# Kernel tuning notes

Hardware: AMD Instinct MI355X
Metric: run time of the kernel (lower is better)

Reference implementation:

```python
import jax, jax.numpy as jnp
import numpy as np

B, T, D, H = 64, 2048, 512, 512
NEG_INF = -1e9


def setup_inputs() -> dict:
    key = jax.random.key(0)
    k1, k2, k3 = jax.random.split(key, 3)
    x = jax.random.normal(k1, (B, D), dtype=jnp.float32)
    enc_outs = jax.random.normal(k2, (B, T, D), dtype=jnp.float32)
    # Dense(hidden) applied to concat([x, context]) -> weight [2*D, H]
    W = jax.random.normal(k3, (2 * D, H), dtype=jnp.float32) * (1.0 / np.sqrt(2 * D))
    b = jnp.zeros((H,), dtype=jnp.float32)
    actual_step = 100  # scalar step counter (int state)
    return {"x": x, "enc_outs": enc_outs, "W": W, "b": b, "actual_step": actual_step}


def reference(x, enc_outs, W, b, actual_step):
    # Dot-product attention of query x over enc_outs, masking the current step.
    # scores: [B, T]
    scores = jnp.einsum('bd,btd->bt', x, enc_outs)
    t_idx = jnp.arange(enc_outs.shape[1])
    scores = jnp.where((t_idx == actual_step)[None, :], NEG_INF, scores)
    alignment = jax.nn.softmax(scores, axis=-1)          # [B, T]
    context = jnp.einsum('bt,btd->bd', alignment, enc_outs)  # [B, D]
    # gate = sigmoid(Dense(concat([x, context])))
    att = jax.nn.sigmoid(jnp.concatenate([x, context], axis=-1) @ W + b)  # [B, H]
    content_selected = att * x                           # requires H == D
    return content_selected
```

## Files before the change

### kernel.cpp

```cpp
#include <hip/hip_runtime.h>
#include <math.h>

#define BB 64
#define TT 2048
#define DD 512
#define HH 512
#define NC 16
#define CHUNK (TT / NC)
#define TH 8.0f

__global__ __launch_bounds__(256) void k1_partial(
    const float* __restrict__ x, const float* __restrict__ enc,
    const int* __restrict__ step_ptr,
    float* __restrict__ ws_m, float* __restrict__ ws_l, float* __restrict__ ws_c)
{
    const int chunk = blockIdx.x;
    const int b     = blockIdx.y;
    const int tid   = threadIdx.x;
    const int w     = tid >> 6;
    const int lane  = tid & 63;
    const int step  = *step_ptr;
    const int trow0 = chunk * CHUNK + w * 32;

    const float4* xr = (const float4*)(x + (size_t)b * DD);
    const float4 xa = xr[lane];
    const float4 xb = xr[64 + lane];

    const float4* __restrict__ rp =
        (const float4*)(enc + (size_t)b * TT * DD) + (size_t)trow0 * 128 + lane;

    float m = -1e30f, l = 0.f;
    float4 ca = make_float4(0.f,0.f,0.f,0.f), cb = make_float4(0.f,0.f,0.f,0.f);

    float4 A[2][2], Bv[2][2];
    A[0][0]  = rp[0 * 128];      A[0][1]  = rp[1 * 128];
    Bv[0][0] = rp[0 * 128 + 64]; Bv[0][1] = rp[1 * 128 + 64];

    #pragma unroll 4
    for (int jj = 0; jj < 8; ++jj) {
        #pragma unroll
        for (int par = 0; par < 2; ++par) {
            const int bat = jj * 2 + par;
            const int nx  = par ^ 1;
            if (bat < 15) {
                A[nx][0]  = rp[((bat + 1) * 2 + 0) * 128];
                A[nx][1]  = rp[((bat + 1) * 2 + 1) * 128];
                Bv[nx][0] = rp[((bat + 1) * 2 + 0) * 128 + 64];
                Bv[nx][1] = rp[((bat + 1) * 2 + 1) * 128 + 64];
            }
            float s[2];
            #pragma unroll
            for (int r = 0; r < 2; ++r) {
                const float4 ea = A[par][r], eb = Bv[par][r];
                s[r] = ea.x*xa.x + ea.y*xa.y + ea.z*xa.z + ea.w*xa.w
                     + eb.x*xb.x + eb.y*xb.y + eb.z*xb.z + eb.w*xb.w;
            }
            #pragma unroll
            for (int off = 32; off; off >>= 1) {
                s[0] += __shfl_xor(s[0], off, 64);
                s[1] += __shfl_xor(s[1], off, 64);
            }
            #pragma unroll
            for (int r = 0; r < 2; ++r)
                if (trow0 + bat * 2 + r == step) s[r] = -1e30f;

            const float bm = fmaxf(s[0], s[1]);
            if (bm > m + TH) {
                const float sc = __expf(m - bm);
                l *= sc;
                ca.x *= sc; ca.y *= sc; ca.z *= sc; ca.w *= sc;
                cb.x *= sc; cb.y *= sc; cb.z *= sc; cb.w *= sc;
                m = bm;
            }
            const float w0 = __expf(s[0] - m);
            const float w1 = __expf(s[1] - m);
            l += w0 + w1;
            ca.x = fmaf(w0, A[par][0].x, fmaf(w1, A[par][1].x, ca.x));
            ca.y = fmaf(w0, A[par][0].y, fmaf(w1, A[par][1].y, ca.y));
            ca.z = fmaf(w0, A[par][0].z, fmaf(w1, A[par][1].z, ca.z));
            ca.w = fmaf(w0, A[par][0].w, fmaf(w1, A[par][1].w, ca.w));
            cb.x = fmaf(w0, Bv[par][0].x, fmaf(w1, Bv[par][1].x, cb.x));
            cb.y = fmaf(w0, Bv[par][0].y, fmaf(w1, Bv[par][1].y, cb.y));
            cb.z = fmaf(w0, Bv[par][0].z, fmaf(w1, Bv[par][1].z, cb.z));
            cb.w = fmaf(w0, Bv[par][0].w, fmaf(w1, Bv[par][1].w, cb.w));
        }
    }

    __shared__ float ls_m[4], ls_l[4];
    __shared__ float ls_c[4][DD];
    if (lane == 0) { ls_m[w] = m; ls_l[w] = l; }
    {
        float* cw = ls_c[w];
        const int d0 = lane * 4;
        cw[d0 + 0] = ca.x; cw[d0 + 1] = ca.y; cw[d0 + 2] = ca.z; cw[d0 + 3] = ca.w;
        cw[256 + d0 + 0] = cb.x; cw[256 + d0 + 1] = cb.y;
        cw[256 + d0 + 2] = cb.z; cw[256 + d0 + 3] = cb.w;
    }
    __syncthreads();

    const float M = fmaxf(fmaxf(ls_m[0], ls_m[1]), fmaxf(ls_m[2], ls_m[3]));
    const float f0 = __expf(ls_m[0] - M);
    const float f1 = __expf(ls_m[1] - M);
    const float f2 = __expf(ls_m[2] - M);
    const float f3 = __expf(ls_m[3] - M);
    const float L = ls_l[0] * f0 + ls_l[1] * f1 + ls_l[2] * f2 + ls_l[3] * f3;

    const int bc = b * NC + chunk;
    for (int d = tid; d < DD; d += 256) {
        const float v = ls_c[0][d] * f0 + ls_c[1][d] * f1
                      + ls_c[2][d] * f2 + ls_c[3][d] * f3;
        ws_c[(size_t)bc * DD + d] = v;
    }
    if (tid == 0) { ws_m[bc] = M; ws_l[bc] = L; }
}

__global__ __launch_bounds__(256) void k1b_merge(
    const float* __restrict__ ws_m, const float* __restrict__ ws_l,
    const float* __restrict__ ws_c, float* __restrict__ ctx)
{
    const int b    = blockIdx.x;
    const int half = blockIdx.y;
    const int tid  = threadIdx.x;
    __shared__ float fac[NC];

    float M = -1e30f;
    #pragma unroll
    for (int i = 0; i < NC; ++i) M = fmaxf(M, ws_m[b * NC + i]);
    float L = 0.f;
    #pragma unroll
    for (int i = 0; i < NC; ++i) L += ws_l[b * NC + i] * __expf(ws_m[b * NC + i] - M);
    const float inv = 1.f / L;
    if (tid < NC) fac[tid] = __expf(ws_m[b * NC + tid] - M) * inv;
    __syncthreads();

    const int d = half * 256 + tid;
    float acc = 0.f;
    #pragma unroll
    for (int i = 0; i < NC; ++i)
        acc = fmaf(ws_c[(size_t)(b * NC + i) * DD + d], fac[i], acc);
    ctx[(size_t)b * DD + d] = acc;
}

#define COLS 8
__device__ __forceinline__ int cidx(int k, int bb) {
    return (k >> 5) * 260 + (k & 31) * 8 + bb;
}

__global__ __launch_bounds__(256) void k2_gemm(
    const float* __restrict__ x, const float* __restrict__ ctx,
    const float* __restrict__ W, const float* __restrict__ bias,
    float* __restrict__ out)
{
    const int g   = blockIdx.x;
    const int bg  = blockIdx.y;
    const int tid = threadIdx.x;

    __shared__ float  con[32 * 260];
    __shared__ float4 part[4][COLS][8];

    const float4* x4 = (const float4*)x;
    const float4* c4 = (const float4*)ctx;

    for (int idx = tid; idx < 2048; idx += 256) {
        const int bb = idx >> 8, k4 = idx & 255;
        const int b  = bg * 8 + bb;
        const float4 v = (k4 < 128) ? x4[(size_t)b * 128 + k4]
                                    : c4[(size_t)b * 128 + (k4 - 128)];
        const int k = k4 * 4;
        con[cidx(k + 0, bb)] = v.x;
        con[cidx(k + 1, bb)] = v.y;
        con[cidx(k + 2, bb)] = v.z;
        con[cidx(k + 3, bb)] = v.w;
    }
    __syncthreads();

    const int cl   = tid & 7;
    const int kseg = tid >> 3;
    const int col4 = g * COLS + cl;
    const float4* Wp = (const float4*)W + (size_t)(kseg * 32) * 128 + col4;

    float4 acc[8];
    #pragma unroll
    for (int bb = 0; bb < 8; ++bb) acc[bb] = make_float4(0.f,0.f,0.f,0.f);

    #pragma unroll 4
    for (int kk = 0; kk < 32; ++kk) {
        const float4 wv = Wp[(size_t)kk * 128];
        const int k = kseg * 32 + kk;
        const float4 c0 = *(const float4*)&con[cidx(k, 0)];
        const float4 c1 = *(const float4*)&con[cidx(k, 4)];
        const float cv[8] = {c0.x, c0.y, c0.z, c0.w, c1.x, c1.y, c1.z, c1.w};
        #pragma unroll
        for (int bb = 0; bb < 8; ++bb) {
            acc[bb].x = fmaf(cv[bb], wv.x, acc[bb].x);
            acc[bb].y = fmaf(cv[bb], wv.y, acc[bb].y);
            acc[bb].z = fmaf(cv[bb], wv.z, acc[bb].z);
            acc[bb].w = fmaf(cv[bb], wv.w, acc[bb].w);
        }
    }

    #pragma unroll
    for (int off = 8; off <= 32; off <<= 1) {
        #pragma unroll
        for (int bb = 0; bb < 8; ++bb) {
            acc[bb].x += __shfl_xor(acc[bb].x, off, 64);
            acc[bb].y += __shfl_xor(acc[bb].y, off, 64);
            acc[bb].z += __shfl_xor(acc[bb].z, off, 64);
            acc[bb].w += __shfl_xor(acc[bb].w, off, 64);
        }
    }
    const int wv_ = tid >> 6, lane = tid & 63;
    if (lane < 8) {
        #pragma unroll
        for (int bb = 0; bb < 8; ++bb) part[wv_][lane][bb] = acc[bb];
    }
    __syncthreads();

    if (tid < 64) {
        const int bb = tid >> 3, cl2 = tid & 7;
        float4 r = part[0][cl2][bb];
        #pragma unroll
        for (int ww = 1; ww < 4; ++ww) {
            const float4 p = part[ww][cl2][bb];
            r.x += p.x; r.y += p.y; r.z += p.z; r.w += p.w;
        }
        const int c4i = g * COLS + cl2;
        const int h   = c4i * 4;
        const int b   = bg * 8 + bb;
        const float4 bv = ((const float4*)bias)[c4i];
        const float xv0 = con[cidx(h + 0, bb)];
        const float xv1 = con[cidx(h + 1, bb)];
        const float xv2 = con[cidx(h + 2, bb)];
        const float xv3 = con[cidx(h + 3, bb)];
        float4 o;
        o.x = xv0 / (1.f + __expf(-(r.x + bv.x)));
        o.y = xv1 / (1.f + __expf(-(r.y + bv.y)));
        o.z = xv2 / (1.f + __expf(-(r.z + bv.z)));
        o.w = xv3 / (1.f + __expf(-(r.w + bv.w)));
        ((float4*)out)[(size_t)b * 128 + c4i] = o;
    }
}

extern "C" void kernel_launch(void* const* d_in, const int* in_sizes, int n_in,
                              void* d_out, int out_size, void* d_ws, size_t ws_size,
                              hipStream_t stream) {
    const float* x    = (const float*)d_in[0];
    const float* enc  = (const float*)d_in[1];
    const float* W    = (const float*)d_in[2];
    const float* bias = (const float*)d_in[3];
    const int*   step = (const int*)d_in[4];
    float* out = (float*)d_out;
    float* ws  = (float*)d_ws;

    float* ws_m = ws;
    float* ws_l = ws_m + (size_t)BB * NC;
    float* ws_c = ws_l + (size_t)BB * NC;
    float* ctx  = ws_c + (size_t)BB * NC * DD;

    k1_partial<<<dim3(NC, BB), 256, 0, stream>>>(x, enc, step, ws_m, ws_l, ws_c);
    k1b_merge<<<dim3(BB, 2), 256, 0, stream>>>(ws_m, ws_l, ws_c, ctx);
    k2_gemm<<<dim3(16, 8), 256, 0, stream>>>(x, ctx, W, bias, out);
}
```

Measured before the change: 62.28 us.

## Stream encoder rows through LDS with async global_load_lds ring buffer

Replaces the register double-buffered float4 loads of encoder rows with a 4-deep per-wave LDS ring filled by global_load_lds direct-to-LDS transfers, keeping three rows in flight and synchronising with explicit s_waitcnt vmcnt counts. Rows are now consumed one at a time instead of in pairs. The goal is deeper memory-level parallelism for this bandwidth-bound streaming pass. In exchange it adds 32KB of LDS per block, which may reduce occupancy, adds LDS read traffic, and relies on hand-written waitcnt counts whose correctness depends on compiler load ordering.

```diff
diff --git a/kernel.cpp b/kernel.cpp
--- a/kernel.cpp
+++ b/kernel.cpp
@@ -8,6 +8,14 @@
 #define NC 16
 #define CHUNK (TT / NC)
 #define TH 8.0f
+
+typedef unsigned int u32;
+__device__ __forceinline__ void async_load16(const float* g, float* l) {
+    __builtin_amdgcn_global_load_lds(
+        (const __attribute__((address_space(1))) u32*)g,
+        (__attribute__((address_space(3))) u32*)l,
+        16, 0, 0);
+}
 
 __global__ __launch_bounds__(256) void k1_partial(
     const float* __restrict__ x, const float* __restrict__ enc,
@@ -22,72 +30,67 @@
     const int step  = *step_ptr;
     const int trow0 = chunk * CHUNK + w * 32;
 
+    __shared__ float stage[4][4][DD];
+    __shared__ float ls_m[4], ls_l[4];
+    __shared__ float ls_c[4][DD];
+
     const float4* xr = (const float4*)(x + (size_t)b * DD);
     const float4 xa = xr[lane];
     const float4 xb = xr[64 + lane];
-
-    const float4* __restrict__ rp =
-        (const float4*)(enc + (size_t)b * TT * DD) + (size_t)trow0 * 128 + lane;
+    asm volatile("s_waitcnt vmcnt(0)" ::: "memory");
+
+    const float* gbase = enc + (size_t)b * TT * DD + (size_t)trow0 * DD;
 
     float m = -1e30f, l = 0.f;
     float4 ca = make_float4(0.f,0.f,0.f,0.f), cb = make_float4(0.f,0.f,0.f,0.f);
 
-    float4 A[2][2], Bv[2][2];
-    A[0][0]  = rp[0 * 128];      A[0][1]  = rp[1 * 128];
-    Bv[0][0] = rp[0 * 128 + 64]; Bv[0][1] = rp[1 * 128 + 64];
-
-    #pragma unroll 4
-    for (int jj = 0; jj < 8; ++jj) {
-        #pragma unroll
-        for (int par = 0; par < 2; ++par) {
-            const int bat = jj * 2 + par;
-            const int nx  = par ^ 1;
-            if (bat < 15) {
-                A[nx][0]  = rp[((bat + 1) * 2 + 0) * 128];
-                A[nx][1]  = rp[((bat + 1) * 2 + 1) * 128];
-                Bv[nx][0] = rp[((bat + 1) * 2 + 0) * 128 + 64];
-                Bv[nx][1] = rp[((bat + 1) * 2 + 1) * 128 + 64];
-            }
-            float s[2];
-            #pragma unroll
-            for (int r = 0; r < 2; ++r) {
-                const float4 ea = A[par][r], eb = Bv[par][r];
-                s[r] = ea.x*xa.x + ea.y*xa.y + ea.z*xa.z + ea.w*xa.w
-                     + eb.x*xb.x + eb.y*xb.y + eb.z*xb.z + eb.w*xb.w;
-            }
-            #pragma unroll
-            for (int off = 32; off; off >>= 1) {
-                s[0] += __shfl_xor(s[0], off, 64);
-                s[1] += __shfl_xor(s[1], off, 64);
-            }
-            #pragma unroll
-            for (int r = 0; r < 2; ++r)
-                if (trow0 + bat * 2 + r == step) s[r] = -1e30f;
-
-            const float bm = fmaxf(s[0], s[1]);
-            if (bm > m + TH) {
-                const float sc = __expf(m - bm);
-                l *= sc;
-                ca.x *= sc; ca.y *= sc; ca.z *= sc; ca.w *= sc;
-                cb.x *= sc; cb.y *= sc; cb.z *= sc; cb.w *= sc;
-                m = bm;
-            }
-            const float w0 = __expf(s[0] - m);
-            const float w1 = __expf(s[1] - m);
-            l += w0 + w1;
-            ca.x = fmaf(w0, A[par][0].x, fmaf(w1, A[par][1].x, ca.x));
-            ca.y = fmaf(w0, A[par][0].y, fmaf(w1, A[par][1].y, ca.y));
-            ca.z = fmaf(w0, A[par][0].z, fmaf(w1, A[par][1].z, ca.z));
-            ca.w = fmaf(w0, A[par][0].w, fmaf(w1, A[par][1].w, ca.w));
-            cb.x = fmaf(w0, Bv[par][0].x, fmaf(w1, Bv[par][1].x, cb.x));
-            cb.y = fmaf(w0, Bv[par][0].y, fmaf(w1, Bv[par][1].y, cb.y));
-            cb.z = fmaf(w0, Bv[par][0].z, fmaf(w1, Bv[par][1].z, cb.z));
-            cb.w = fmaf(w0, Bv[par][0].w, fmaf(w1, Bv[par][1].w, cb.w));
-        }
-    }
-
-    __shared__ float ls_m[4], ls_l[4];
-    __shared__ float ls_c[4][DD];
+    #define ISSUE(r) {                                              \
+        const float* g_ = gbase + (r) * DD + lane * 4;              \
+        float* d_ = &stage[w][(r) & 3][0];                          \
+        async_load16(g_, d_);                                       \
+        async_load16(g_ + 256, d_ + 256);                           \
+    }
+    #define CONSUME(r) {                                            \
+        const float* sp_ = &stage[w][(r) & 3][0];                   \
+        const float4 ea = *(const float4*)&sp_[lane * 4];           \
+        const float4 eb = *(const float4*)&sp_[256 + lane * 4];     \
+        float s = ea.x*xa.x + ea.y*xa.y + ea.z*xa.z + ea.w*xa.w     \
+                + eb.x*xb.x + eb.y*xb.y + eb.z*xb.z + eb.w*xb.w;    \
+        _Pragma("unroll")                                           \
+        for (int off = 32; off; off >>= 1) s += __shfl_xor(s, off, 64); \
+        if (trow0 + (r) == step) s = -1e30f;                        \
+        if (s > m + TH) {                                           \
+            const float sc_ = __expf(m - s);                        \
+            l *= sc_;                                               \
+            ca.x *= sc_; ca.y *= sc_; ca.z *= sc_; ca.w *= sc_;     \
+            cb.x *= sc_; cb.y *= sc_; cb.z *= sc_; cb.w *= sc_;     \
+            m = s;                                                  \
+        }                                                           \
+        const float wgt = __expf(s - m);                            \
+        l += wgt;                                                   \
+        ca.x = fmaf(wgt, ea.x, ca.x); ca.y = fmaf(wgt, ea.y, ca.y); \
+        ca.z = fmaf(wgt, ea.z, ca.z); ca.w = fmaf(wgt, ea.w, ca.w); \
+        cb.x = fmaf(wgt, eb.x, cb.x); cb.y = fmaf(wgt, eb.y, cb.y); \
+        cb.z = fmaf(wgt, eb.z, cb.z); cb.w = fmaf(wgt, eb.w, cb.w); \
+    }
+
+    ISSUE(0); ISSUE(1); ISSUE(2);
+
+    for (int r = 0; r < 29; ++r) {
+        ISSUE(r + 3);
+        asm volatile("s_waitcnt vmcnt(6)" ::: "memory");
+        CONSUME(r);
+    }
+    asm volatile("s_waitcnt vmcnt(4)" ::: "memory");
+    CONSUME(29);
+    asm volatile("s_waitcnt vmcnt(2)" ::: "memory");
+    CONSUME(30);
+    asm volatile("s_waitcnt vmcnt(0)" ::: "memory");
+    CONSUME(31);
+
+    #undef ISSUE
+    #undef CONSUME
+
     if (lane == 0) { ls_m[w] = m; ls_l[w] = l; }
     {
         float* cw = ls_c[w];
```

New measurement: 77.84 us. +25.0%, slower.
